# Kernel tuning notes

Measured on AMD Instinct MI355X. Metric: run time of the kernel, lower is better.

The kernel has to match this reference:

```python
import jax, jax.numpy as jnp
import numpy as np

HIDDEN = 300
ATOM_FDIM = 133
BOND_ONLY_FDIM = 14
BOND_FDIM = ATOM_FDIM + BOND_ONLY_FDIM  # 147, chemprop concatenates atom feats into bond feats
DEPTH = 3
N_ATOMS = 100000
N_BONDS = 200000  # directed bonds, stored as reverse pairs (2k, 2k+1)
MAX_NB = 6
N_MOLS = 2000


def _lin(key, fan_in, fan_out):
    s = 1.0 / np.sqrt(fan_in)
    return jax.random.uniform(key, (fan_in, fan_out), jnp.float32, -s, s)


def setup_inputs() -> dict:
    key = jax.random.key(0)
    ks = jax.random.split(key, 16)
    f_atoms = jax.random.normal(ks[0], (N_ATOMS, ATOM_FDIM), jnp.float32)
    f_bonds = jax.random.normal(ks[1], (N_BONDS, BOND_FDIM), jnp.float32)
    a2b = jax.random.randint(ks[2], (N_ATOMS, MAX_NB), 0, N_BONDS, jnp.int32)
    b2a = jax.random.randint(ks[3], (N_BONDS,), 0, N_ATOMS, jnp.int32)
    b2revb = jnp.arange(N_BONDS, dtype=jnp.int32) ^ 1  # reverse-bond pairing
    graph_idx = jnp.sort(jax.random.randint(ks[4], (N_ATOMS,), 0, N_MOLS, jnp.int32))
    params = dict(
        W_i=_lin(ks[5], BOND_FDIM, HIDDEN),              # no bias in chemprop W_i
        W_h=_lin(ks[6], HIDDEN, HIDDEN),                 # no bias in chemprop W_h
        W_o=_lin(ks[7], ATOM_FDIM + HIDDEN, HIDDEN),
        b_o=jnp.zeros((HIDDEN,), jnp.float32),
        W_node=_lin(ks[8], HIDDEN, ATOM_FDIM),
        b_node=jnp.zeros((ATOM_FDIM,), jnp.float32),
        W_edge=_lin(ks[9], HIDDEN, BOND_ONLY_FDIM),
        b_edge=jnp.zeros((BOND_ONLY_FDIM,), jnp.float32),
        W_g1=_lin(ks[10], HIDDEN, HIDDEN),
        b_g1=jnp.zeros((HIDDEN,), jnp.float32),
        W_g2=_lin(ks[11], HIDDEN, 1),
        b_g2=jnp.zeros((1,), jnp.float32),
    )
    return dict(f_atoms=f_atoms, f_bonds=f_bonds, a2b=a2b, b2a=b2a,
                b2revb=b2revb, graph_idx=graph_idx, **params)


def reference(f_atoms, f_bonds, a2b, b2a, b2revb, graph_idx,
              W_i, W_h, W_o, b_o, W_node, b_node,
              W_edge, b_edge, W_g1, b_g1, W_g2, b_g2):
    # ---- chemprop bond-message MPN encoder (dropout=0) ----
    inp = f_bonds @ W_i                       # [n_bonds, H]
    msg = jax.nn.relu(inp)
    for _ in range(DEPTH - 1):
        a_msg = msg[a2b].sum(axis=1)          # gather neighbor bond msgs -> [n_atoms, H]
        msg = jax.nn.relu(inp + (a_msg[b2a] - msg[b2revb]) @ W_h)
    a_msg = msg[a2b].sum(axis=1)
    atom_hiddens = jax.nn.relu(jnp.concatenate([f_atoms, a_msg], axis=-1) @ W_o + b_o)
    # ---- graph pooling: per-molecule SUM (as in the forward loop) ----
    graph_emb = jax.ops.segment_sum(atom_hiddens, graph_idx, num_segments=N_MOLS)
    # ---- heads ----
    node_preds = atom_hiddens @ W_node + b_node
    # bond loop: visits each reverse pair once (even bond first), averages endpoint atoms
    e1 = jnp.arange(0, N_BONDS, 2)
    a1 = b2a[e1]
    a2 = b2a[b2revb[e1]]
    h_avg = 0.5 * (atom_hiddens[a1] + atom_hiddens[a2])
    edge_preds = h_avg @ W_edge + b_edge
    graph_preds = jax.nn.relu(graph_emb @ W_g1 + b_g1) @ W_g2 + b_g2
    return node_preds, edge_preds, graph_preds
```

## Files before the change

kernel.cpp:

```cpp
#include <hip/hip_runtime.h>

typedef unsigned short u16;
typedef unsigned int u32;

#define N_ATOMS 100000
#define N_BONDS 200000
#define N_EDGES 100000
#define HIDDEN 300
#define HP 320
#define ATOM_FDIM 133
#define BOND_FDIM 147
#define CATP 448
#define N_MOLS 2000

typedef __bf16 bf16x8 __attribute__((ext_vector_type(8)));
typedef float f32x4 __attribute__((ext_vector_type(4)));

__device__ __forceinline__ u16 f2bf(float f) {
    union { float f; u32 u; } x; x.f = f;
    u32 u = x.u;
    u32 r = u + 0x7fffu + ((u >> 16) & 1u);
    return (u16)(r >> 16);
}
__device__ __forceinline__ float bf2f(u16 h) {
    union { u32 u; float f; } x; x.u = ((u32)h) << 16;
    return x.f;
}

union U8 { uint4 v; u16 h[8]; };
union U4 { uint2 v; u16 h[4]; };

#define GL16(gp, lp) __builtin_amdgcn_global_load_lds( \
    (const __attribute__((address_space(1))) u32*)(gp), \
    (__attribute__((address_space(3))) u32*)(lp), 16, 0, 0)

template<int EP, int KSTEPS, int LDA, int NB>
__global__ __launch_bounds__(256, 4) void k_gemmG(
    const u16* __restrict__ A, int M,
    const u16* __restrict__ Bt, int ldb, int Nout,
    const float* __restrict__ bias, const float* __restrict__ bias2,
    u16* __restrict__ O1, float* __restrict__ F1, float* __restrict__ F2,
    const u16* __restrict__ inp_in, int nwg)
{
    __shared__ __align__(16) u16 SM[128 * 32 + 64 * 32];
    u16* As = SM;
    u16* Bs = SM + 128 * 32;

    const int bid = blockIdx.x;
    const int q = nwg >> 3, r = nwg & 7;
    const int xcd = bid & 7, sidx = bid >> 3;
    const int wg = (xcd < r ? xcd * (q + 1) : r * (q + 1) + (xcd - r) * q) + sidx;

    const int n0 = (wg % NB) * 64;
    const int row0 = (wg / NB) * 128;

    const int tid = threadIdx.x;
    const int lane = tid & 63;
    const int wv = tid >> 6;
    const int wr = wv >> 1, wc = wv & 1;
    const int lrow = lane & 15;
    const int g = lane >> 4;

    const int lr = lane >> 2, lc = lane & 3;
    int arow0 = row0 + wv * 32 + lr;
    int arow1 = arow0 + 16;
    if (arow0 >= M) arow0 = M - 1;
    if (arow1 >= M) arow1 = M - 1;
    const u16* gA0 = A + (size_t)arow0 * LDA + lc * 8;
    const u16* gA1 = A + (size_t)arow1 * LDA + lc * 8;
    const u16* gB  = Bt + (size_t)(n0 + wv * 16 + lr) * ldb + lc * 8;
    u16* lA0 = &As[(wv * 32) * 32];
    u16* lA1 = &As[(wv * 32 + 16) * 32];
    u16* lB  = &Bs[(wv * 16) * 32];

    U4 ii[8];
    if constexpr (EP == 2) {
#pragma unroll
        for (int m = 0; m < 4; m++) {
            const int row = row0 + wr * 64 + m * 16 + lrow;
#pragma unroll
            for (int n = 0; n < 2; n++) {
                if (row < M)
                    ii[m * 2 + n].v = *(const uint2*)&inp_in[
                        (size_t)row * HP + n0 + wc * 32 + n * 16 + g * 4];
            }
        }
    }

    f32x4 acc[4][2] = {};

#pragma unroll
    for (int ks = 0; ks < KSTEPS; ks++) {
        const int k0 = ks * 32;
        GL16(gA0 + k0, lA0);
        GL16(gA1 + k0, lA1);
        GL16(gB + k0, lB);
        __syncthreads();
        bf16x8 af[4], bfr[2];
#pragma unroll
        for (int m = 0; m < 4; m++)
            af[m] = *(const bf16x8*)&As[(wr * 64 + m * 16 + lrow) * 32 + g * 8];
#pragma unroll
        for (int n = 0; n < 2; n++)
            bfr[n] = *(const bf16x8*)&Bs[(wc * 32 + n * 16 + lrow) * 32 + g * 8];
#pragma unroll
        for (int m = 0; m < 4; m++)
#pragma unroll
            for (int n = 0; n < 2; n++)
                acc[m][n] = __builtin_amdgcn_mfma_f32_16x16x32_bf16(bfr[n], af[m], acc[m][n], 0, 0, 0);
        __syncthreads();
    }

    if constexpr (EP == 4) {
        float* LDSf = (float*)SM;
#pragma unroll
        for (int m = 0; m < 4; m++) {
            __syncthreads();
#pragma unroll
            for (int n = 0; n < 2; n++)
                *(f32x4*)&LDSf[(size_t)(wr * 16 + lrow) * 68 + wc * 32 + n * 16 + g * 4] = acc[m][n];
            __syncthreads();
#pragma unroll
            for (int i = 0; i < 8; i++) {
                const int rl = wv + i * 4;
                const int grow = row0 + ((rl & 16) ? 64 : 0) + m * 16 + (rl & 15);
                const float v = LDSf[(size_t)rl * 68 + lane];
                const int col = n0 + lane;
                if (grow < M) {
                    if (col < 133) F1[(size_t)grow * 133 + col] = v + bias[col];
                    else if (col < 147) F2[(size_t)grow * 16 + (col - 133)] = v + bias2[col - 133];
                }
            }
        }
    } else {
#pragma unroll
        for (int m = 0; m < 4; m++) {
            const int row = row0 + wr * 64 + m * 16 + lrow;
            if (row >= M) continue;
#pragma unroll
            for (int n = 0; n < 2; n++) {
                const int colb = n0 + wc * 32 + n * 16 + g * 4;
                U4 o;
                if constexpr (EP == 1) {
#pragma unroll
                    for (int qq = 0; qq < 4; qq++) o.h[qq] = f2bf(acc[m][n][qq]);
                } else if constexpr (EP == 2) {
#pragma unroll
                    for (int qq = 0; qq < 4; qq++) o.h[qq] = f2bf(acc[m][n][qq] + bf2f(ii[m * 2 + n].h[qq]));
                } else {
#pragma unroll
                    for (int qq = 0; qq < 4; qq++) {
                        float x = acc[m][n][qq] + ((colb + qq) < Nout ? bias[colb + qq] : 0.f);
                        o.h[qq] = f2bf(fmaxf(x, 0.f));
                    }
                }
                *(uint2*)&O1[(size_t)row * HP + colb] = o.v;
            }
        }
    }
}

__global__ void k_pack_wt(const float* __restrict__ W, u16* __restrict__ Bt,
                          int K, int N, int Kp, int Np)
{
    int idx = blockIdx.x * 256 + threadIdx.x;
    if (idx >= Np * Kp) return;
    int n = idx / Kp, k = idx - n * Kp;
    Bt[idx] = (n < N && k < K) ? f2bf(W[(size_t)k * N + n]) : (u16)0;
}

__global__ void k_pack_wo(const float* __restrict__ W, u16* __restrict__ Bt)
{
    int idx = blockIdx.x * 256 + threadIdx.x;
    if (idx >= 320 * CATP) return;
    int n = idx / CATP, k = idx - n * CATP;
    float v = 0.f;
    if (n < HIDDEN) {
        if (k < HIDDEN) v = W[(size_t)(ATOM_FDIM + k) * HIDDEN + n];
        else if (k >= 304 && k < 304 + ATOM_FDIM) v = W[(size_t)(k - 304) * HIDDEN + n];
    }
    Bt[idx] = f2bf(v);
}

__global__ void k_pack_wne(const float* __restrict__ Wn, const float* __restrict__ We,
                           u16* __restrict__ Bt)
{
    int idx = blockIdx.x * 256 + threadIdx.x;
    if (idx >= 320 * 320) return;
    int n = idx / 320, k = idx - n * 320;
    float v = 0.f;
    if (k < HIDDEN) {
        if (n < ATOM_FDIM) v = Wn[(size_t)k * ATOM_FDIM + n];
        else if (n < ATOM_FDIM + 14) v = We[(size_t)k * 14 + (n - ATOM_FDIM)];
    }
    Bt[idx] = f2bf(v);
}

__global__ __launch_bounds__(256) void k_pack_bonds(const float* __restrict__ fb, u16* __restrict__ out)
{
    int idx = blockIdx.x * 256 + threadIdx.x;
    if (idx >= N_BONDS * 20) return;
    int b = idx / 20, c0 = (idx - b * 20) * 8;
    U8 u;
#pragma unroll
    for (int e = 0; e < 8; e++) {
        int col = c0 + e;
        u.h[e] = (col < BOND_FDIM) ? f2bf(fb[(size_t)b * BOND_FDIM + col]) : (u16)0;
    }
    *(uint4*)&out[(size_t)b * 160 + c0] = u.v;
}

__global__ __launch_bounds__(256) void k_cat_fa(const float* __restrict__ fa, u16* __restrict__ cat)
{
    int idx = blockIdx.x * 256 + threadIdx.x;
    if (idx >= N_ATOMS * 18) return;
    int a = idx / 18, c0 = 304 + (idx - a * 18) * 8;
    U8 u;
#pragma unroll
    for (int e = 0; e < 8; e++) {
        int fc = c0 + e - 304;
        u.h[e] = (fc < ATOM_FDIM) ? f2bf(fa[(size_t)a * ATOM_FDIM + fc]) : (u16)0;
    }
    *(uint4*)&cat[(size_t)a * CATP + c0] = u.v;
}

template<int OST>
__global__ __launch_bounds__(256) void k_aggregate(const u16* __restrict__ h,
    const int* __restrict__ a2b, u16* __restrict__ amsg)
{
    int idx = blockIdx.x * 256 + threadIdx.x;
    if (idx >= N_ATOMS * 40) return;
    int a = idx / 40, c = (idx - a * 40) * 8;
    float s[8] = {};
#pragma unroll
    for (int j = 0; j < 6; j++) {
        int b = a2b[a * 6 + j];
        U8 u; u.v = *(const uint4*)&h[(size_t)b * HP + c];
#pragma unroll
        for (int i = 0; i < 8; i++) s[i] += fmaxf(bf2f(u.h[i]), 0.f);
    }
    U8 o;
#pragma unroll
    for (int i = 0; i < 8; i++) o.h[i] = f2bf(s[i]);
    *(uint4*)&amsg[(size_t)a * OST + c] = o.v;
}

__global__ __launch_bounds__(256) void k_delta(const u16* __restrict__ amsg,
    const u16* __restrict__ h, const int* __restrict__ b2a, u16* __restrict__ dlt)
{
    int idx = blockIdx.x * 256 + threadIdx.x;
    if (idx >= N_BONDS * 40) return;
    int b = idx / 40, c = (idx - b * 40) * 8;
    int a = b2a[b];
    U8 x; x.v = *(const uint4*)&amsg[(size_t)a * HP + c];
    U8 y; y.v = *(const uint4*)&h[(size_t)(b ^ 1) * HP + c];
    U8 o;
#pragma unroll
    for (int i = 0; i < 8; i++)
        o.h[i] = f2bf(bf2f(x.h[i]) - fmaxf(bf2f(y.h[i]), 0.f));
    *(uint4*)&dlt[(size_t)b * HP + c] = o.v;
}

__global__ __launch_bounds__(256) void k_edge(const float* __restrict__ E,
    const int* __restrict__ b2a, float* __restrict__ out)
{
    int idx = blockIdx.x * 256 + threadIdx.x;
    if (idx >= N_EDGES * 7) return;
    int e = idx / 7, p = idx - e * 7;
    int a1 = b2a[2 * e], a2 = b2a[2 * e + 1];
    float2 x = *(const float2*)&E[(size_t)a1 * 16 + 2 * p];
    float2 y = *(const float2*)&E[(size_t)a2 * 16 + 2 * p];
    float2 o; o.x = 0.5f * (x.x + y.x); o.y = 0.5f * (x.y + y.y);
    *(float2*)&out[(size_t)e * 14 + 2 * p] = o;
}

__device__ __forceinline__ int lower_bound_i(const int* a, int n, int v) {
    int lo = 0, hi = n;
    while (lo < hi) { int mid = (lo + hi) >> 1; if (a[mid] < v) lo = mid + 1; else hi = mid; }
    return lo;
}
__global__ __launch_bounds__(320) void k_segsum(const u16* __restrict__ ah,
    const int* __restrict__ gidx, float* __restrict__ gemb)
{
    int g = blockIdx.x;
    int c = threadIdx.x;
    int s = lower_bound_i(gidx, N_ATOMS, g);
    int e = lower_bound_i(gidx, N_ATOMS, g + 1);
    float sum = 0.f;
    for (int a = s; a < e; a++) sum += bf2f(ah[(size_t)a * HP + c]);
    gemb[(size_t)g * HP + c] = sum;
}

__global__ __launch_bounds__(320) void k_g1(const float* __restrict__ gemb,
    const float* __restrict__ W, const float* __restrict__ b, float* __restrict__ gh)
{
    int g = blockIdx.x, j = threadIdx.x;
    float acc = 0.f;
    if (j < HIDDEN) {
        acc = b[j];
        for (int k = 0; k < HIDDEN; k++)
            acc = fmaf(gemb[(size_t)g * HP + k], W[(size_t)k * HIDDEN + j], acc);
        acc = fmaxf(acc, 0.f);
    }
    gh[(size_t)g * HP + j] = (j < HIDDEN) ? acc : 0.f;
}
__global__ __launch_bounds__(64) void k_g2(const float* __restrict__ gh,
    const float* __restrict__ W, const float* __restrict__ b, float* __restrict__ out)
{
    int g = blockIdx.x, l = threadIdx.x;
    float acc = 0.f;
    for (int j = l; j < HIDDEN; j += 64) acc += gh[(size_t)g * HP + j] * W[j];
#pragma unroll
    for (int off = 32; off; off >>= 1) acc += __shfl_down(acc, off, 64);
    if (l == 0) out[g] = acc + b[0];
}

extern "C" void kernel_launch(void* const* d_in, const int* in_sizes, int n_in,
                              void* d_out, int out_size, void* d_ws, size_t ws_size,
                              hipStream_t stream)
{
    const float* f_atoms = (const float*)d_in[0];
    const float* f_bonds = (const float*)d_in[1];
    const int* a2b    = (const int*)d_in[2];
    const int* b2a    = (const int*)d_in[3];
    const int* gidx   = (const int*)d_in[5];
    const float* W_i    = (const float*)d_in[6];
    const float* W_h    = (const float*)d_in[7];
    const float* W_o    = (const float*)d_in[8];
    const float* b_o    = (const float*)d_in[9];
    const float* W_node = (const float*)d_in[10];
    const float* b_node = (const float*)d_in[11];
    const float* W_edge = (const float*)d_in[12];
    const float* b_edge = (const float*)d_in[13];
    const float* W_g1   = (const float*)d_in[14];
    const float* b_g1   = (const float*)d_in[15];
    const float* W_g2   = (const float*)d_in[16];
    const float* b_g2   = (const float*)d_in[17];

    char* ws = (char*)d_ws;
    u16* inp   = (u16*)(ws + 0);
    u16* hA    = (u16*)(ws + 128000000);
    u16* hB    = (u16*)(ws + 256000000);
    u16* amsg  = (u16*)(ws + 384000000);
    u16* wt_i  = (u16*)(ws + 448000000);
    u16* wt_h  = (u16*)(ws + 448200000);
    u16* wt_o  = (u16*)(ws + 448500000);
    u16* wt_ne = (u16*)(ws + 448800000);
    float* gemb = (float*)(ws + 449300000);
    float* gh   = (float*)(ws + 452000000);

    float* out_node  = (float*)d_out;
    float* out_edge  = out_node + (size_t)N_ATOMS * ATOM_FDIM;
    float* out_graph = out_node + 14700000;

    dim3 blk(256);

    k_pack_wt<<<(320 * 160 + 255) / 256, blk, 0, stream>>>(W_i, wt_i, BOND_FDIM, HIDDEN, 160, 320);
    k_pack_wt<<<(320 * 320 + 255) / 256, blk, 0, stream>>>(W_h, wt_h, HIDDEN, HIDDEN, 320, 320);
    k_pack_wo<<<(320 * CATP + 255) / 256, blk, 0, stream>>>(W_o, wt_o);
    k_pack_wne<<<(320 * 320 + 255) / 256, blk, 0, stream>>>(W_node, W_edge, wt_ne);

    const int mbB = (N_BONDS + 127) / 128;
    const int mbA = (N_ATOMS + 127) / 128;
    const int gAg = (N_ATOMS * 40 + 255) / 256;
    const int gDl = (N_BONDS * 40 + 255) / 256;
    const int nwgI = 5 * mbB;
    const int nwgO = 5 * mbA;
    const int nwgH = 3 * mbA;

    u16* fb16 = hA;
    k_pack_bonds<<<(N_BONDS * 20 + 255) / 256, blk, 0, stream>>>(f_bonds, fb16);

    k_gemmG<1, 5, 160, 5><<<nwgI, blk, 0, stream>>>(
        fb16, N_BONDS, wt_i, 160, 0, nullptr, nullptr,
        inp, nullptr, nullptr, nullptr, nwgI);

    const u16* hcur = inp;
    for (int d = 0; d < 2; ++d) {
        k_aggregate<HP><<<gAg, blk, 0, stream>>>(hcur, a2b, amsg);
        k_delta<<<gDl, blk, 0, stream>>>(amsg, hcur, b2a, hB);
        k_gemmG<2, 10, 320, 5><<<nwgI, blk, 0, stream>>>(
            hB, N_BONDS, wt_h, 320, 0, nullptr, nullptr,
            hA, nullptr, nullptr, inp, nwgI);
        hcur = hA;
    }

    u16* catbuf = inp;
    k_aggregate<CATP><<<gAg, blk, 0, stream>>>(hcur, a2b, catbuf);
    k_cat_fa<<<(N_ATOMS * 18 + 255) / 256, blk, 0, stream>>>(f_atoms, catbuf);

    u16* ah = hB;
    k_gemmG<3, 14, 448, 5><<<nwgO, blk, 0, stream>>>(
        catbuf, N_ATOMS, wt_o, CATP, HIDDEN, b_o, nullptr,
        ah, nullptr, nullptr, nullptr, nwgO);

    float* Ebuf = (float*)amsg;
    k_gemmG<4, 10, 320, 3><<<nwgH, blk, 0, stream>>>(
        ah, N_ATOMS, wt_ne, 320, 0, b_node, b_edge,
        nullptr, out_node, Ebuf, nwgH ? nullptr : nullptr, nwgH);

    k_edge<<<(N_EDGES * 7 + 255) / 256, blk, 0, stream>>>(Ebuf, b2a, out_edge);

    k_segsum<<<N_MOLS, 320, 0, stream>>>(ah, gidx, gemb);
    k_g1<<<N_MOLS, 320, 0, stream>>>(gemb, W_g1, b_g1, gh);
    k_g2<<<N_MOLS, 64, 0, stream>>>(gh, W_g2, b_g2, out_graph);
}
```

Before: 1.006 ms.

## Triple-buffer GEMM LDS tiles with async global-to-LDS prefetch two steps ahead

Replaces the single-buffered LDS staging in the shared GEMM kernel with a three-stage ring. Direct global-to-LDS loads are issued two K-steps ahead, and partial vmcnt waits let the MFMA work on one stage overlap the loads of the next two. LDS use grows from 12 KB to 36 KB per block, which may limit occupancy at the requested four blocks per SM. The ordering also now relies on hand-written waitcnt and barrier sequencing.

```diff
diff --git a/kernel.cpp b/kernel.cpp
--- a/kernel.cpp
+++ b/kernel.cpp
@@ -42,9 +42,7 @@
     u16* __restrict__ O1, float* __restrict__ F1, float* __restrict__ F2,
     const u16* __restrict__ inp_in, int nwg)
 {
-    __shared__ __align__(16) u16 SM[128 * 32 + 64 * 32];
-    u16* As = SM;
-    u16* Bs = SM + 128 * 32;
+    __shared__ __align__(16) u16 SM[3 * 6144];
 
     const int bid = blockIdx.x;
     const int q = nwg >> 3, r = nwg & 7;
@@ -69,9 +67,6 @@
     const u16* gA0 = A + (size_t)arow0 * LDA + lc * 8;
     const u16* gA1 = A + (size_t)arow1 * LDA + lc * 8;
     const u16* gB  = Bt + (size_t)(n0 + wv * 16 + lr) * ldb + lc * 8;
-    u16* lA0 = &As[(wv * 32) * 32];
-    u16* lA1 = &As[(wv * 32 + 16) * 32];
-    u16* lB  = &Bs[(wv * 16) * 32];
 
     U4 ii[8];
     if constexpr (EP == 2) {
@@ -87,28 +82,46 @@
         }
     }
 
+    auto STAGE = [&](int p, int ks) {
+        const int k0 = ks * 32;
+        u16* base = SM + p * 6144;
+        GL16(gA0 + k0, base + wv * 1024);
+        GL16(gA1 + k0, base + wv * 1024 + 512);
+        GL16(gB  + k0, base + 4096 + wv * 512);
+    };
+
     f32x4 acc[4][2] = {};
 
+    STAGE(0, 0);
+    if constexpr (KSTEPS > 1) STAGE(1, 1);
+
 #pragma unroll
     for (int ks = 0; ks < KSTEPS; ks++) {
-        const int k0 = ks * 32;
-        GL16(gA0 + k0, lA0);
-        GL16(gA1 + k0, lA1);
-        GL16(gB + k0, lB);
-        __syncthreads();
+        if (ks + 2 < KSTEPS) STAGE((ks + 2) % 3, ks + 2);
+        if (ks + 2 < KSTEPS)      asm volatile("s_waitcnt vmcnt(6)" ::: "memory");
+        else if (ks + 1 < KSTEPS) asm volatile("s_waitcnt vmcnt(3)" ::: "memory");
+        else                      asm volatile("s_waitcnt vmcnt(0)" ::: "memory");
+        __builtin_amdgcn_s_barrier();
+        asm volatile("" ::: "memory");
+
+        const u16* Asp = SM + (ks % 3) * 6144;
+        const u16* Bsp = Asp + 4096;
         bf16x8 af[4], bfr[2];
 #pragma unroll
         for (int m = 0; m < 4; m++)
-            af[m] = *(const bf16x8*)&As[(wr * 64 + m * 16 + lrow) * 32 + g * 8];
+            af[m] = *(const bf16x8*)&Asp[(wr * 64 + m * 16 + lrow) * 32 + g * 8];
 #pragma unroll
         for (int n = 0; n < 2; n++)
-            bfr[n] = *(const bf16x8*)&Bs[(wc * 32 + n * 16 + lrow) * 32 + g * 8];
+            bfr[n] = *(const bf16x8*)&Bsp[(wc * 32 + n * 16 + lrow) * 32 + g * 8];
 #pragma unroll
         for (int m = 0; m < 4; m++)
 #pragma unroll
             for (int n = 0; n < 2; n++)
                 acc[m][n] = __builtin_amdgcn_mfma_f32_16x16x32_bf16(bfr[n], af[m], acc[m][n], 0, 0, 0);
-        __syncthreads();
+
+        asm volatile("" ::: "memory");
+        __builtin_amdgcn_s_barrier();
+        asm volatile("" ::: "memory");
     }
 
     if constexpr (EP == 4) {
@@ -397,7 +410,7 @@
     float* Ebuf = (float*)amsg;
     k_gemmG<4, 10, 320, 3><<<nwgH, blk, 0, stream>>>(
         ah, N_ATOMS, wt_ne, 320, 0, b_node, b_edge,
-        nullptr, out_node, Ebuf, nwgH ? nullptr : nullptr, nwgH);
+        nullptr, out_node, Ebuf, nullptr, nwgH);
 
     k_edge<<<(N_EDGES * 7 + 255) / 256, blk, 0, stream>>>(Ebuf, b2a, out_edge);
 
```

Measured after the change: 1.033 ms. 2.7% more time.

## Fuse delta gather into W_h GEMM via dual MFMA with negated weights

Applied to the files above, without the earlier changes.

Removes the separate k_delta kernel. The W_h GEMM now gathers amsg rows by b2a and the reverse-bond msg rows directly into LDS, and computes amsg@W - msg_rev@W as two MFMAs, the second using sign-flipped weights. The first GEMM writes both the raw inp and relu(inp), so the aggregate no longer applies relu, and the atom-feature concat is folded into the final aggregate kernel. This saves a full bond-sized write/read pass and a few launches, at the cost of double MFMA work, more LDS per block and uncoalesced gathered A loads inside the GEMM.

```diff
diff --git a/kernel.cpp b/kernel.cpp
--- a/kernel.cpp
+++ b/kernel.cpp
@@ -34,17 +34,18 @@
     (const __attribute__((address_space(1))) u32*)(gp), \
     (__attribute__((address_space(3))) u32*)(lp), 16, 0, 0)
 
-template<int EP, int KSTEPS, int LDA, int NB>
+template<int DSRC, int EP, int KSTEPS, int LDA, int NB>
 __global__ __launch_bounds__(256, 4) void k_gemmG(
-    const u16* __restrict__ A, int M,
+    const u16* __restrict__ A, const u16* __restrict__ Y,
+    const int* __restrict__ i1, int M,
     const u16* __restrict__ Bt, int ldb, int Nout,
     const float* __restrict__ bias, const float* __restrict__ bias2,
-    u16* __restrict__ O1, float* __restrict__ F1, float* __restrict__ F2,
+    u16* __restrict__ O1, u16* __restrict__ O2,
+    float* __restrict__ F1, float* __restrict__ F2,
     const u16* __restrict__ inp_in, int nwg)
 {
-    __shared__ __align__(16) u16 SM[128 * 32 + 64 * 32];
-    u16* As = SM;
-    u16* Bs = SM + 128 * 32;
+    constexpr int SMU = (DSRC == 2) ? 10240 : 6144;
+    __shared__ __align__(16) u16 SM[SMU];
 
     const int bid = blockIdx.x;
     const int q = nwg >> 3, r = nwg & 7;
@@ -66,15 +67,24 @@
     int arow1 = arow0 + 16;
     if (arow0 >= M) arow0 = M - 1;
     if (arow1 >= M) arow1 = M - 1;
-    const u16* gA0 = A + (size_t)arow0 * LDA + lc * 8;
-    const u16* gA1 = A + (size_t)arow1 * LDA + lc * 8;
-    const u16* gB  = Bt + (size_t)(n0 + wv * 16 + lr) * ldb + lc * 8;
-    u16* lA0 = &As[(wv * 32) * 32];
-    u16* lA1 = &As[(wv * 32 + 16) * 32];
-    u16* lB  = &Bs[(wv * 16) * 32];
+
+    const u16* gA0; const u16* gA1;
+    const u16* gY0 = nullptr; const u16* gY1 = nullptr;
+    if constexpr (DSRC == 2) {
+        gA0 = A + (size_t)i1[arow0] * HP + lc * 8;
+        gA1 = A + (size_t)i1[arow1] * HP + lc * 8;
+        gY0 = Y + (size_t)(arow0 ^ 1) * HP + lc * 8;
+        gY1 = Y + (size_t)(arow1 ^ 1) * HP + lc * 8;
+    } else {
+        gA0 = A + (size_t)arow0 * LDA + lc * 8;
+        gA1 = A + (size_t)arow1 * LDA + lc * 8;
+    }
+    const u16* gB = Bt + (size_t)(n0 + wv * 16 + lr) * ldb + lc * 8;
+
+    constexpr int BOFF = (DSRC == 2) ? 8192 : 4096;
 
     U4 ii[8];
-    if constexpr (EP == 2) {
+    if constexpr (EP == 5) {
 #pragma unroll
         for (int m = 0; m < 4; m++) {
             const int row = row0 + wr * 64 + m * 16 + lrow;
@@ -92,22 +102,51 @@
 #pragma unroll
     for (int ks = 0; ks < KSTEPS; ks++) {
         const int k0 = ks * 32;
-        GL16(gA0 + k0, lA0);
-        GL16(gA1 + k0, lA1);
-        GL16(gB + k0, lB);
+        GL16(gA0 + k0, SM + wv * 1024);
+        GL16(gA1 + k0, SM + wv * 1024 + 512);
+        if constexpr (DSRC == 2) {
+            GL16(gY0 + k0, SM + 4096 + wv * 1024);
+            GL16(gY1 + k0, SM + 4096 + wv * 1024 + 512);
+        }
+        GL16(gB + k0, SM + BOFF + wv * 512);
         __syncthreads();
-        bf16x8 af[4], bfr[2];
+
+        bf16x8 bfr[2];
+#pragma unroll
+        for (int n = 0; n < 2; n++)
+            bfr[n] = *(const bf16x8*)&SM[BOFF + (wc * 32 + n * 16 + lrow) * 32 + g * 8];
+
+        bf16x8 af[4];
 #pragma unroll
         for (int m = 0; m < 4; m++)
-            af[m] = *(const bf16x8*)&As[(wr * 64 + m * 16 + lrow) * 32 + g * 8];
-#pragma unroll
-        for (int n = 0; n < 2; n++)
-            bfr[n] = *(const bf16x8*)&Bs[(wc * 32 + n * 16 + lrow) * 32 + g * 8];
-#pragma unroll
-        for (int m = 0; m < 4; m++)
-#pragma unroll
-            for (int n = 0; n < 2; n++)
-                acc[m][n] = __builtin_amdgcn_mfma_f32_16x16x32_bf16(bfr[n], af[m], acc[m][n], 0, 0, 0);
+            af[m] = *(const bf16x8*)&SM[(wr * 64 + m * 16 + lrow) * 32 + g * 8];
+
+        if constexpr (DSRC == 2) {
+            bf16x8 yf[4], bneg[2];
+#pragma unroll
+            for (int m = 0; m < 4; m++)
+                yf[m] = *(const bf16x8*)&SM[4096 + (wr * 64 + m * 16 + lrow) * 32 + g * 8];
+#pragma unroll
+            for (int n = 0; n < 2; n++) {
+                uint4 bu = *(uint4*)&bfr[n];
+                bu.x ^= 0x80008000u; bu.y ^= 0x80008000u;
+                bu.z ^= 0x80008000u; bu.w ^= 0x80008000u;
+                bneg[n] = *(bf16x8*)&bu;
+            }
+#pragma unroll
+            for (int m = 0; m < 4; m++)
+#pragma unroll
+                for (int n = 0; n < 2; n++) {
+                    acc[m][n] = __builtin_amdgcn_mfma_f32_16x16x32_bf16(bfr[n], af[m], acc[m][n], 0, 0, 0);
+                    acc[m][n] = __builtin_amdgcn_mfma_f32_16x16x32_bf16(bneg[n], yf[m], acc[m][n], 0, 0, 0);
+                }
+        } else {
+#pragma unroll
+            for (int m = 0; m < 4; m++)
+#pragma unroll
+                for (int n = 0; n < 2; n++)
+                    acc[m][n] = __builtin_amdgcn_mfma_f32_16x16x32_bf16(bfr[n], af[m], acc[m][n], 0, 0, 0);
+        }
         __syncthreads();
     }
 
@@ -144,17 +183,29 @@
                 if constexpr (EP == 1) {
 #pragma unroll
                     for (int qq = 0; qq < 4; qq++) o.h[qq] = f2bf(acc[m][n][qq]);
-                } else if constexpr (EP == 2) {
-#pragma unroll
-                    for (int qq = 0; qq < 4; qq++) o.h[qq] = f2bf(acc[m][n][qq] + bf2f(ii[m * 2 + n].h[qq]));
+                    *(uint2*)&O1[(size_t)row * HP + colb] = o.v;
+                } else if constexpr (EP == 5) {
+#pragma unroll
+                    for (int qq = 0; qq < 4; qq++)
+                        o.h[qq] = f2bf(fmaxf(acc[m][n][qq] + bf2f(ii[m * 2 + n].h[qq]), 0.f));
+                    *(uint2*)&O1[(size_t)row * HP + colb] = o.v;
+                } else if constexpr (EP == 6) {
+                    U4 o2;
+#pragma unroll
+                    for (int qq = 0; qq < 4; qq++) {
+                        o.h[qq] = f2bf(acc[m][n][qq]);
+                        o2.h[qq] = f2bf(fmaxf(acc[m][n][qq], 0.f));
+                    }
+                    *(uint2*)&O1[(size_t)row * HP + colb] = o.v;
+                    *(uint2*)&O2[(size_t)row * HP + colb] = o2.v;
                 } else {
 #pragma unroll
                     for (int qq = 0; qq < 4; qq++) {
                         float x = acc[m][n][qq] + ((colb + qq) < Nout ? bias[colb + qq] : 0.f);
                         o.h[qq] = f2bf(fmaxf(x, 0.f));
                     }
+                    *(uint2*)&O1[(size_t)row * HP + colb] = o.v;
                 }
-                *(uint2*)&O1[(size_t)row * HP + colb] = o.v;
             }
         }
     }
@@ -210,55 +261,39 @@
     *(uint4*)&out[(size_t)b * 160 + c0] = u.v;
 }
 
-__global__ __launch_bounds__(256) void k_cat_fa(const float* __restrict__ fa, u16* __restrict__ cat)
-{
-    int idx = blockIdx.x * 256 + threadIdx.x;
-    if (idx >= N_ATOMS * 18) return;
-    int a = idx / 18, c0 = 304 + (idx - a * 18) * 8;
-    U8 u;
-#pragma unroll
-    for (int e = 0; e < 8; e++) {
-        int fc = c0 + e - 304;
-        u.h[e] = (fc < ATOM_FDIM) ? f2bf(fa[(size_t)a * ATOM_FDIM + fc]) : (u16)0;
-    }
-    *(uint4*)&cat[(size_t)a * CATP + c0] = u.v;
-}
-
-template<int OST>
-__global__ __launch_bounds__(256) void k_aggregate(const u16* __restrict__ h,
-    const int* __restrict__ a2b, u16* __restrict__ amsg)
-{
-    int idx = blockIdx.x * 256 + threadIdx.x;
-    if (idx >= N_ATOMS * 40) return;
-    int a = idx / 40, c = (idx - a * 40) * 8;
+template<int OST, int FA>
+__global__ __launch_bounds__(256) void k_aggregate(const u16* __restrict__ msg,
+    const int* __restrict__ a2b, const float* __restrict__ fa, u16* __restrict__ out)
+{
+    constexpr int CH = FA ? 56 : 40;
+    int idx = blockIdx.x * 256 + threadIdx.x;
+    if (idx >= N_ATOMS * CH) return;
+    int a = idx / CH, cc = idx - a * CH;
+    if (FA && cc >= 38) {
+        int c0 = cc * 8 + (38 * 8 == 304 ? 0 : 0);
+        c0 = cc * 8;
+        U8 u;
+#pragma unroll
+        for (int e = 0; e < 8; e++) {
+            int fc = c0 + e - 304;
+            u.h[e] = (fc >= 0 && fc < ATOM_FDIM) ? f2bf(fa[(size_t)a * ATOM_FDIM + fc]) : (u16)0;
+        }
+        *(uint4*)&out[(size_t)a * OST + c0] = u.v;
+        return;
+    }
+    int c = cc * 8;
     float s[8] = {};
 #pragma unroll
     for (int j = 0; j < 6; j++) {
         int b = a2b[a * 6 + j];
-        U8 u; u.v = *(const uint4*)&h[(size_t)b * HP + c];
-#pragma unroll
-        for (int i = 0; i < 8; i++) s[i] += fmaxf(bf2f(u.h[i]), 0.f);
+        U8 u; u.v = *(const uint4*)&msg[(size_t)b * HP + c];
+#pragma unroll
+        for (int i = 0; i < 8; i++) s[i] += bf2f(u.h[i]);
     }
     U8 o;
 #pragma unroll
     for (int i = 0; i < 8; i++) o.h[i] = f2bf(s[i]);
-    *(uint4*)&amsg[(size_t)a * OST + c] = o.v;
-}
-
-__global__ __launch_bounds__(256) void k_delta(const u16* __restrict__ amsg,
-    const u16* __restrict__ h, const int* __restrict__ b2a, u16* __restrict__ dlt)
-{
-    int idx = blockIdx.x * 256 + threadIdx.x;
-    if (idx >= N_BONDS * 40) return;
-    int b = idx / 40, c = (idx - b * 40) * 8;
-    int a = b2a[b];
-    U8 x; x.v = *(const uint4*)&amsg[(size_t)a * HP + c];
-    U8 y; y.v = *(const uint4*)&h[(size_t)(b ^ 1) * HP + c];
-    U8 o;
-#pragma unroll
-    for (int i = 0; i < 8; i++)
-        o.h[i] = f2bf(bf2f(x.h[i]) - fmaxf(bf2f(y.h[i]), 0.f));
-    *(uint4*)&dlt[(size_t)b * HP + c] = o.v;
+    *(uint4*)&out[(size_t)a * OST + c] = o.v;
 }
 
 __global__ __launch_bounds__(256) void k_edge(const float* __restrict__ E,
@@ -339,8 +374,8 @@
 
     char* ws = (char*)d_ws;
     u16* inp   = (u16*)(ws + 0);
-    u16* hA    = (u16*)(ws + 128000000);
-    u16* hB    = (u16*)(ws + 256000000);
+    u16* msgA  = (u16*)(ws + 128000000);
+    u16* msgB  = (u16*)(ws + 256000000);
     u16* amsg  = (u16*)(ws + 384000000);
     u16* wt_i  = (u16*)(ws + 448000000);
     u16* wt_h  = (u16*)(ws + 448200000);
@@ -363,41 +398,43 @@
     const int mbB = (N_BONDS + 127) / 128;
     const int mbA = (N_ATOMS + 127) / 128;
     const int gAg = (N_ATOMS * 40 + 255) / 256;
-    const int gDl = (N_BONDS * 40 + 255) / 256;
+    const int gAgF = (N_ATOMS * 56 + 255) / 256;
     const int nwgI = 5 * mbB;
     const int nwgO = 5 * mbA;
     const int nwgH = 3 * mbA;
 
-    u16* fb16 = hA;
+    u16* fb16 = msgB;
     k_pack_bonds<<<(N_BONDS * 20 + 255) / 256, blk, 0, stream>>>(f_bonds, fb16);
 
-    k_gemmG<1, 5, 160, 5><<<nwgI, blk, 0, stream>>>(
-        fb16, N_BONDS, wt_i, 160, 0, nullptr, nullptr,
-        inp, nullptr, nullptr, nullptr, nwgI);
-
-    const u16* hcur = inp;
-    for (int d = 0; d < 2; ++d) {
-        k_aggregate<HP><<<gAg, blk, 0, stream>>>(hcur, a2b, amsg);
-        k_delta<<<gDl, blk, 0, stream>>>(amsg, hcur, b2a, hB);
-        k_gemmG<2, 10, 320, 5><<<nwgI, blk, 0, stream>>>(
-            hB, N_BONDS, wt_h, 320, 0, nullptr, nullptr,
-            hA, nullptr, nullptr, inp, nwgI);
-        hcur = hA;
-    }
+    u16* msg1 = msgA;
+    k_gemmG<0, 6, 5, 160, 5><<<nwgI, blk, 0, stream>>>(
+        fb16, nullptr, nullptr, N_BONDS, wt_i, 160, 0, nullptr, nullptr,
+        inp, msg1, nullptr, nullptr, nullptr, nwgI);
+
+    k_aggregate<HP, 0><<<gAg, blk, 0, stream>>>(msg1, a2b, nullptr, amsg);
+    u16* msg2 = msgB;
+    k_gemmG<2, 5, 10, HP, 5><<<nwgI, blk, 0, stream>>>(
+        amsg, msg1, b2a, N_BONDS, wt_h, 320, 0, nullptr, nullptr,
+        msg2, nullptr, nullptr, nullptr, inp, nwgI);
+
+    k_aggregate<HP, 0><<<gAg, blk, 0, stream>>>(msg2, a2b, nullptr, amsg);
+    u16* msg3 = msgA;
+    k_gemmG<2, 5, 10, HP, 5><<<nwgI, blk, 0, stream>>>(
+        amsg, msg2, b2a, N_BONDS, wt_h, 320, 0, nullptr, nullptr,
+        msg3, nullptr, nullptr, nullptr, inp, nwgI);
 
     u16* catbuf = inp;
-    k_aggregate<CATP><<<gAg, blk, 0, stream>>>(hcur, a2b, catbuf);
-    k_cat_fa<<<(N_ATOMS * 18 + 255) / 256, blk, 0, stream>>>(f_atoms, catbuf);
-
-    u16* ah = hB;
-    k_gemmG<3, 14, 448, 5><<<nwgO, blk, 0, stream>>>(
-        catbuf, N_ATOMS, wt_o, CATP, HIDDEN, b_o, nullptr,
-        ah, nullptr, nullptr, nullptr, nwgO);
+    k_aggregate<CATP, 1><<<gAgF, blk, 0, stream>>>(msg3, a2b, f_atoms, catbuf);
+
+    u16* ah = msgB;
+    k_gemmG<0, 3, 14, 448, 5><<<nwgO, blk, 0, stream>>>(
+        catbuf, nullptr, nullptr, N_ATOMS, wt_o, CATP, HIDDEN, b_o, nullptr,
+        ah, nullptr, nullptr, nullptr, nullptr, nwgO);
 
     float* Ebuf = (float*)amsg;
-    k_gemmG<4, 10, 320, 3><<<nwgH, blk, 0, stream>>>(
-        ah, N_ATOMS, wt_ne, 320, 0, b_node, b_edge,
-        nullptr, out_node, Ebuf, nwgH ? nullptr : nullptr, nwgH);
+    k_gemmG<0, 4, 10, HP, 3><<<nwgH, blk, 0, stream>>>(
+        ah, nullptr, nullptr, N_ATOMS, wt_ne, 320, 0, b_node, b_edge,
+        nullptr, nullptr, out_node, Ebuf, nullptr, nwgH);
 
     k_edge<<<(N_EDGES * 7 + 255) / 256, blk, 0, stream>>>(Ebuf, b2a, out_edge);
 
```

Measured after the change: 970.7 us. 1.04x faster.
